# Performance work log

Measured on AMD Instinct MI355X. Metric: run time of the kernel, lower is better.

## Reference

```python
import jax, jax.numpy as jnp
import numpy as np

B, CAP, H, NH = 128, 65536, 512, 8
HD = H // NH
GH = H // 4  # gate hidden


def setup_inputs() -> dict:
    key = jax.random.key(0)
    ks = jax.random.split(key, 8)
    s = 1.0 / np.sqrt(H)
    sg = 1.0 / np.sqrt(GH)
    return {
        "query": jax.random.normal(ks[0], (B, H), jnp.float32),
        "memory_keys": jax.random.normal(ks[1], (CAP, H), jnp.float32) * s,
        "memory_values": jax.random.normal(ks[2], (CAP, H), jnp.float32) * s,
        "in_proj_w": jax.random.normal(ks[3], (3 * H, H), jnp.float32) * s,
        "in_proj_b": jnp.zeros((3 * H,), jnp.float32),
        "out_proj_w": jax.random.normal(ks[4], (H, H), jnp.float32) * s,
        "out_proj_b": jnp.zeros((H,), jnp.float32),
        "gate_w1": jax.random.normal(ks[5], (GH, H), jnp.float32) * s,
        "gate_b1": jnp.zeros((GH,), jnp.float32),
        "gate_w2": jax.random.normal(ks[6], (1, GH), jnp.float32) * sg,
        "gate_b2": jnp.zeros((1,), jnp.float32),
        "usage_count": jnp.zeros((CAP,), jnp.float32),
        "last_used": jnp.zeros((CAP,), jnp.float32),
        "step_counter": 1,
    }


def reference(query, memory_keys, memory_values, in_proj_w, in_proj_b,
              out_proj_w, out_proj_b, gate_w1, gate_b1, gate_w2, gate_b2,
              usage_count, last_used, step_counter):
    # nn.MultiheadAttention packed projections: rows [0:H]=Wq, [H:2H]=Wk, [2H:3H]=Wv
    wq, wk, wv = in_proj_w[:H], in_proj_w[H:2 * H], in_proj_w[2 * H:]
    bq, bk, bv = in_proj_b[:H], in_proj_b[H:2 * H], in_proj_b[2 * H:]

    q = (query @ wq.T + bq).reshape(B, NH, HD)           # [B, h, d] (q_len = 1)
    k = (memory_keys @ wk.T + bk).reshape(CAP, NH, HD)   # [C, h, d]
    v = (memory_values @ wv.T + bv).reshape(CAP, NH, HD)  # [C, h, d]

    scores = jnp.einsum('bhd,chd->bhc', q, k) / np.sqrt(HD)  # [B, h, C]
    attn = jax.nn.softmax(scores, axis=-1)
    ctx = jnp.einsum('bhc,chd->bhd', attn, v).reshape(B, H)
    attn_out = ctx @ out_proj_w.T + out_proj_b               # [B, H]

    # usage bookkeeping: attn_weights averaged over heads, then over batch
    avg_attn = attn.mean(axis=(0, 1))                        # [C]
    new_usage = usage_count + avg_attn
    new_last = jnp.where(avg_attn > 1e-3,
                         jnp.float32(step_counter), last_used)

    # gating MLP: Linear -> ReLU -> Linear -> Sigmoid
    gate = jax.nn.sigmoid(
        jax.nn.relu(query @ gate_w1.T + gate_b1) @ gate_w2.T + gate_b2)  # [B, 1]
    memory_output = gate * attn_out                          # [B, H]
    return memory_output, new_usage, new_last
```

## Files before the change

### kernel.cpp

```cpp
#include <hip/hip_runtime.h>
#include <stdint.h>


typedef __bf16 b16x8 __attribute__((ext_vector_type(8)));
typedef float f32x4 __attribute__((ext_vector_type(4)));

static __device__ __forceinline__ unsigned short f2bf(float f) {
  return __builtin_bit_cast(unsigned short, (__bf16)f);
}

static __device__ __forceinline__ f32x4 MFMA(b16x8 a, b16x8 b, f32x4 c) {
  return __builtin_amdgcn_mfma_f32_16x16x32_bf16(a, b, c, 0, 0, 0);
}

#define GLL16(g, l)                                                          \
  __builtin_amdgcn_global_load_lds(                                          \
      (const __attribute__((address_space(1))) void*)(g),                    \
      (__attribute__((address_space(3))) void*)(l), 16, 0, 0)

#define SBAR() __builtin_amdgcn_sched_barrier(0)

__global__ void k_convert_w(const float* __restrict__ w, unsigned short* __restrict__ dst) {
  int i = blockIdx.x * 256 + threadIdx.x;
  float4 v = reinterpret_cast<const float4*>(w + 512 * 512)[i];
  ushort4 o;
  o.x = f2bf(v.x); o.y = f2bf(v.y); o.z = f2bf(v.z); o.w = f2bf(v.w);
  reinterpret_cast<ushort4*>(dst)[i] = o;
}

__global__ void k_proj_q(const float* __restrict__ query, const float* __restrict__ w,
                         const float* __restrict__ bias, unsigned short* __restrict__ qout) {
  __shared__ float qs[512];
  int b = blockIdx.x, j = threadIdx.x;
  qs[j] = query[b * 512 + j];
  __syncthreads();
  float acc = bias[j];
  const float4* q4 = reinterpret_cast<const float4*>(qs);
  const float4* w4 = reinterpret_cast<const float4*>(w + j * 512);
#pragma unroll 8
  for (int i = 0; i < 128; ++i) {
    float4 a = q4[i], c = w4[i];
    acc += a.x * c.x + a.y * c.y + a.z * c.z + a.w * c.w;
  }
  qout[b * 512 + j] = f2bf(acc);
}

__global__ void k_gate(const float* __restrict__ query, const float* __restrict__ w1,
                       const float* __restrict__ b1, const float* __restrict__ w2,
                       const float* __restrict__ b2, float* __restrict__ gate) {
  __shared__ float qs[512];
  __shared__ float red[2];
  int b = blockIdx.x, j = threadIdx.x;
  qs[j] = query[b * 512 + j];
  qs[j + 128] = query[b * 512 + j + 128];
  qs[j + 256] = query[b * 512 + j + 256];
  qs[j + 384] = query[b * 512 + j + 384];
  __syncthreads();
  float acc = b1[j];
  const float4* q4 = reinterpret_cast<const float4*>(qs);
  const float4* w4 = reinterpret_cast<const float4*>(w1 + j * 512);
#pragma unroll 8
  for (int i = 0; i < 128; ++i) {
    float4 a = q4[i], c = w4[i];
    acc += a.x * c.x + a.y * c.y + a.z * c.z + a.w * c.w;
  }
  float t = fmaxf(acc, 0.f) * w2[j];
#pragma unroll
  for (int off = 1; off < 64; off <<= 1) t += __shfl_xor(t, off, 64);
  if ((j & 63) == 0) red[j >> 6] = t;
  __syncthreads();
  if (j == 0) {
    float z = red[0] + red[1] + b2[0];
    gate[b] = 1.f / (1.f + __builtin_amdgcn_exp2f(-z * 1.44269504088896f));
  }
}

__global__ __launch_bounds__(256, 2) void k_proj_kv(
    const float* __restrict__ mk, const float* __restrict__ mv,
    const unsigned short* __restrict__ wkb, const unsigned short* __restrict__ wvb,
    const float* __restrict__ in_b,
    unsigned short* __restrict__ kout, unsigned short* __restrict__ vtout) {
  const int p = blockIdx.x;
  const int xcd = p & 7, slot = p >> 3;
  const int isV = xcd >> 2;
  const int j0 = (slot & 3) * 128;
  const int c0 = (xcd & 3) * 16384 + (slot >> 2) * 128;
  const float* Ag = isV ? mv : mk;
  const unsigned short* W = isV ? wvb : wkb;
  const float* bias = in_b + (isV ? 1024 : 512);
  const int tid = threadIdx.x;
  const int w = tid >> 6;
  const int wr = w >> 1, wc = w & 1;
  const int ln = tid & 15, g = (tid & 63) >> 4;
  const int lane = tid & 63;

  __shared__ __align__(16) float          AL[3][128 * 32];
  __shared__ __align__(16) unsigned short WL[2][128 * 32];

  f32x4 acc[4][4];
#pragma unroll
  for (int m = 0; m < 4; ++m)
#pragma unroll
    for (int n = 0; n < 4; ++n) acc[m][n] = {0.f, 0.f, 0.f, 0.f};

  const float* srcA[4];
  int dstA[4];
#pragma unroll
  for (int i = 0; i < 4; ++i) {
    int row = i * 32 + w * 8 + (lane >> 3);
    int cs = (lane & 7) ^ (row & 7);
    srcA[i] = Ag + (size_t)(c0 + row) * 512 + cs * 4;
    dstA[i] = (i * 256 + w * 64) * 4;
  }
  const unsigned short* srcW[2];
  int dstW[2];
#pragma unroll
  for (int i = 0; i < 2; ++i) {
    int row = i * 64 + w * 16 + (lane >> 2);
    int cs = (lane & 3) ^ ((row >> 1) & 3);
    srcW[i] = W + (size_t)(j0 + row) * 512 + cs * 8;
    dstW[i] = (i * 256 + w * 64) * 8;
  }

  GLL16(srcW[0], &WL[0][dstW[0]]);
  GLL16(srcW[1], &WL[0][dstW[1]]);
#pragma unroll
  for (int i = 0; i < 4; ++i) GLL16(srcA[i], &AL[0][dstA[i]]);
#pragma unroll
  for (int i = 0; i < 4; ++i) GLL16(srcA[i] + 32, &AL[1][dstA[i]]);
  SBAR();
  asm volatile("s_waitcnt vmcnt(4)" ::: "memory");
  SBAR();
  __builtin_amdgcn_s_barrier();
  SBAR();

#pragma unroll
  for (int kk = 0; kk < 16; ++kk) {
    const int a = kk % 3;
    const int bwl = kk & 1;
    const int k1 = (kk < 15) ? kk + 1 : 15;
    const int k2 = (kk < 14) ? kk + 2 : 15;
    GLL16(srcW[0] + k1 * 32, &WL[bwl ^ 1][dstW[0]]);
    GLL16(srcW[1] + k1 * 32, &WL[bwl ^ 1][dstW[1]]);
#pragma unroll
    for (int i = 0; i < 4; ++i) GLL16(srcA[i] + k2 * 32, &AL[(kk + 2) % 3][dstA[i]]);
    SBAR();
    b16x8 af[4], wf[4];
#pragma unroll
    for (int m = 0; m < 4; ++m) {
      int r = 64 * wr + 16 * m + ln;
      f32x4 lo = *reinterpret_cast<const f32x4*>(&AL[a][r * 32 + (((2 * g) ^ (r & 7)) << 2)]);
      f32x4 hi = *reinterpret_cast<const f32x4*>(&AL[a][r * 32 + (((2 * g + 1) ^ (r & 7)) << 2)]);
      b16x8 v;
      v[0] = (__bf16)lo[0]; v[1] = (__bf16)lo[1]; v[2] = (__bf16)lo[2]; v[3] = (__bf16)lo[3];
      v[4] = (__bf16)hi[0]; v[5] = (__bf16)hi[1]; v[6] = (__bf16)hi[2]; v[7] = (__bf16)hi[3];
      af[m] = v;
    }
#pragma unroll
    for (int n = 0; n < 4; ++n) {
      int r = 64 * wc + 16 * n + ln;
      wf[n] = *reinterpret_cast<const b16x8*>(&WL[bwl][r * 32 + ((g ^ ((r >> 1) & 3)) << 3)]);
    }
    if (!isV) {
#pragma unroll
      for (int m = 0; m < 4; ++m)
#pragma unroll
        for (int n = 0; n < 4; ++n) acc[m][n] = MFMA(wf[n], af[m], acc[m][n]);
    } else {
#pragma unroll
      for (int m = 0; m < 4; ++m)
#pragma unroll
        for (int n = 0; n < 4; ++n) acc[m][n] = MFMA(af[m], wf[n], acc[m][n]);
    }
    SBAR();
    asm volatile("s_waitcnt vmcnt(4) lgkmcnt(0)" ::: "memory");
    SBAR();
    __builtin_amdgcn_s_barrier();
    SBAR();
  }
  asm volatile("s_waitcnt vmcnt(0)" ::: "memory");

  if (!isV) {
#pragma unroll
    for (int m = 0; m < 4; ++m) {
      int c = c0 + 64 * wr + 16 * m + ln;
#pragma unroll
      for (int n = 0; n < 4; ++n) {
        int jb = j0 + 64 * wc + 16 * n + 4 * g;
        float4 bb = *reinterpret_cast<const float4*>(&bias[jb]);
        ushort4 o;
        o.x = f2bf(acc[m][n][0] + bb.x);
        o.y = f2bf(acc[m][n][1] + bb.y);
        o.z = f2bf(acc[m][n][2] + bb.z);
        o.w = f2bf(acc[m][n][3] + bb.w);
        *reinterpret_cast<ushort4*>(&kout[(size_t)c * 512 + jb]) = o;
      }
    }
  } else {
#pragma unroll
    for (int n = 0; n < 4; ++n) {
      int j = j0 + 64 * wc + 16 * n + ln;
      float bj = bias[j];
#pragma unroll
      for (int m = 0; m < 4; ++m) {
        int cb = c0 + 64 * wr + 16 * m + 4 * g;
        ushort4 o;
        o.x = f2bf(acc[m][n][0] + bj);
        o.y = f2bf(acc[m][n][1] + bj);
        o.z = f2bf(acc[m][n][2] + bj);
        o.w = f2bf(acc[m][n][3] + bj);
        *reinterpret_cast<ushort4*>(&vtout[(size_t)j * 65536 + cb]) = o;
      }
    }
  }
}

__global__ __launch_bounds__(256) void k_attn1(
    const unsigned short* __restrict__ kb, const unsigned short* __restrict__ vt,
    const unsigned short* __restrict__ qb,
    float* __restrict__ l_ws, float* __restrict__ ctxT) {
  const int h = blockIdx.y, cg = blockIdx.x;
  const int tid = threadIdx.x;
  const int wv = tid >> 6, wr = wv >> 1, wc = wv & 1;
  const int ln = tid & 15, g = (tid & 63) >> 4;
  __shared__ __align__(16) unsigned short kS[128 * 64];
  __shared__ __align__(16) unsigned short pS[128 * 128];
  __shared__ __align__(16) unsigned short vS[64 * 128];
  const float SC = 0.125f * 1.44269504088896f;

  b16x8 qf[4][2];
#pragma unroll
  for (int n = 0; n < 4; ++n)
#pragma unroll
    for (int ks = 0; ks < 2; ++ks) {
      int b = 64 * wc + 16 * n + ln;
      qf[n][ks] = *reinterpret_cast<const b16x8*>(&qb[(size_t)b * 512 + h * 64 + ks * 32 + g * 8]);
    }
  f32x4 pacc[2][4];
#pragma unroll
  for (int m = 0; m < 2; ++m)
#pragma unroll
    for (int n = 0; n < 4; ++n) pacc[m][n] = {0.f, 0.f, 0.f, 0.f};
  float lsum[4] = {0.f, 0.f, 0.f, 0.f};

  for (int it = 0; it < 8; ++it) {
    int c0g = cg * 1024 + it * 128;
#pragma unroll
    for (int i = 0; i < 4; ++i) {
      int fl = i * 256 + tid, row = fl >> 3, p8 = fl & 7;
      uint4 d = *reinterpret_cast<const uint4*>(&kb[(size_t)(c0g + row) * 512 + h * 64 + p8 * 8]);
      *reinterpret_cast<uint4*>(&kS[(row * 8 + (p8 ^ (row & 7))) * 8]) = d;
    }
#pragma unroll
    for (int i = 0; i < 4; ++i) {
      int fl = i * 256 + tid, row = fl >> 4, p16 = fl & 15;
      uint4 d = *reinterpret_cast<const uint4*>(&vt[(size_t)(h * 64 + row) * 65536 + c0g + p16 * 8]);
      *reinterpret_cast<uint4*>(&vS[(row * 16 + (p16 ^ (row & 7))) * 8]) = d;
    }
    __syncthreads();

    f32x4 sacc[4][4];
#pragma unroll
    for (int m = 0; m < 4; ++m)
#pragma unroll
      for (int n = 0; n < 4; ++n) sacc[m][n] = {0.f, 0.f, 0.f, 0.f};
#pragma unroll
    for (int ks = 0; ks < 2; ++ks) {
      b16x8 a[4];
#pragma unroll
      for (int m = 0; m < 4; ++m) {
        int row = 64 * wr + 16 * m + ln;
        a[m] = *reinterpret_cast<const b16x8*>(&kS[(row * 8 + ((ks * 4 + g) ^ (row & 7))) * 8]);
      }
#pragma unroll
      for (int m = 0; m < 4; ++m)
#pragma unroll
        for (int n = 0; n < 4; ++n) sacc[m][n] = MFMA(a[m], qf[n][ks], sacc[m][n]);
    }
#pragma unroll
    for (int m = 0; m < 4; ++m)
#pragma unroll
      for (int n = 0; n < 4; ++n) {
        float p0 = __builtin_amdgcn_exp2f(sacc[m][n][0] * SC);
        float p1 = __builtin_amdgcn_exp2f(sacc[m][n][1] * SC);
        float p2 = __builtin_amdgcn_exp2f(sacc[m][n][2] * SC);
        float p3 = __builtin_amdgcn_exp2f(sacc[m][n][3] * SC);
        lsum[n] += (p0 + p1) + (p2 + p3);
        int b = 64 * wc + 16 * n + ln;
        int c = 64 * wr + 16 * m + 4 * g;
        int base = b * 128 + (((c >> 3) ^ (b & 7)) * 8) + (c & 7);
        ushort2 lo, hi;
        lo.x = f2bf(p0); lo.y = f2bf(p1);
        hi.x = f2bf(p2); hi.y = f2bf(p3);
        *reinterpret_cast<ushort2*>(&pS[base]) = lo;
        *reinterpret_cast<ushort2*>(&pS[base + 2]) = hi;
      }
    __syncthreads();
#pragma unroll
    for (int ks = 0; ks < 4; ++ks) {
      b16x8 av[2], bp[4];
#pragma unroll
      for (int m = 0; m < 2; ++m) {
        int row = 32 * wr + 16 * m + ln;
        av[m] = *reinterpret_cast<const b16x8*>(&vS[(row * 16 + ((ks * 4 + g) ^ (row & 7))) * 8]);
      }
#pragma unroll
      for (int n = 0; n < 4; ++n) {
        int row = 64 * wc + 16 * n + ln;
        bp[n] = *reinterpret_cast<const b16x8*>(&pS[(row * 16 + ((ks * 4 + g) ^ (row & 7))) * 8]);
      }
#pragma unroll
      for (int m = 0; m < 2; ++m)
#pragma unroll
        for (int n = 0; n < 4; ++n) pacc[m][n] = MFMA(av[m], bp[n], pacc[m][n]);
    }
    __syncthreads();
  }
#pragma unroll
  for (int n = 0; n < 4; ++n) {
    float v = lsum[n];
    v += __shfl_xor(v, 16, 64);
    v += __shfl_xor(v, 32, 64);
    if ((tid & 63) < 16) atomicAdd(&l_ws[h * 128 + 64 * wc + 16 * n + ln], v);
  }
#pragma unroll
  for (int m = 0; m < 2; ++m)
#pragma unroll
    for (int n = 0; n < 4; ++n)
#pragma unroll
      for (int r = 0; r < 4; ++r) {
        int d = 32 * wr + 16 * m + 4 * g + r;
        int b = 64 * wc + 16 * n + ln;
        atomicAdd(&ctxT[(h * 64 + d) * 128 + b], pacc[m][n][r]);
      }
}

__global__ __launch_bounds__(256) void k_attn2(
    const unsigned short* __restrict__ kb, const unsigned short* __restrict__ qb,
    const float* __restrict__ l_ws, float* __restrict__ avgA) {
  const int h = blockIdx.y, cg = blockIdx.x;
  const int tid = threadIdx.x;
  const int wv = tid >> 6, wr = wv >> 1, wc = wv & 1;
  const int ln = tid & 15, g = (tid & 63) >> 4;
  __shared__ __align__(16) unsigned short kS[128 * 64];
  __shared__ float wS[128];
  const float SC = 0.125f * 1.44269504088896f;
  if (tid < 128) wS[tid] = 1.f / l_ws[h * 128 + tid];
  b16x8 qf[4][2];
#pragma unroll
  for (int n = 0; n < 4; ++n)
#pragma unroll
    for (int ks = 0; ks < 2; ++ks) {
      int b = 64 * wc + 16 * n + ln;
      qf[n][ks] = *reinterpret_cast<const b16x8*>(&qb[(size_t)b * 512 + h * 64 + ks * 32 + g * 8]);
    }
  __syncthreads();
  float wn[4];
#pragma unroll
  for (int n = 0; n < 4; ++n) wn[n] = wS[64 * wc + 16 * n + ln];

  for (int it = 0; it < 8; ++it) {
    int c0g = cg * 1024 + it * 128;
#pragma unroll
    for (int i = 0; i < 4; ++i) {
      int fl = i * 256 + tid, row = fl >> 3, p8 = fl & 7;
      uint4 d = *reinterpret_cast<const uint4*>(&kb[(size_t)(c0g + row) * 512 + h * 64 + p8 * 8]);
      *reinterpret_cast<uint4*>(&kS[(row * 8 + (p8 ^ (row & 7))) * 8]) = d;
    }
    __syncthreads();
    f32x4 sacc[4][4];
#pragma unroll
    for (int m = 0; m < 4; ++m)
#pragma unroll
      for (int n = 0; n < 4; ++n) sacc[m][n] = {0.f, 0.f, 0.f, 0.f};
#pragma unroll
    for (int ks = 0; ks < 2; ++ks) {
      b16x8 a[4];
#pragma unroll
      for (int m = 0; m < 4; ++m) {
        int row = 64 * wr + 16 * m + ln;
        a[m] = *reinterpret_cast<const b16x8*>(&kS[(row * 8 + ((ks * 4 + g) ^ (row & 7))) * 8]);
      }
#pragma unroll
      for (int m = 0; m < 4; ++m)
#pragma unroll
        for (int n = 0; n < 4; ++n) sacc[m][n] = MFMA(a[m], qf[n][ks], sacc[m][n]);
    }
#pragma unroll
    for (int m = 0; m < 4; ++m) {
      float s0 = 0.f, s1 = 0.f, s2 = 0.f, s3 = 0.f;
#pragma unroll
      for (int n = 0; n < 4; ++n) {
        s0 += __builtin_amdgcn_exp2f(sacc[m][n][0] * SC) * wn[n];
        s1 += __builtin_amdgcn_exp2f(sacc[m][n][1] * SC) * wn[n];
        s2 += __builtin_amdgcn_exp2f(sacc[m][n][2] * SC) * wn[n];
        s3 += __builtin_amdgcn_exp2f(sacc[m][n][3] * SC) * wn[n];
      }
#pragma unroll
      for (int off = 1; off < 16; off <<= 1) {
        s0 += __shfl_xor(s0, off, 64);
        s1 += __shfl_xor(s1, off, 64);
        s2 += __shfl_xor(s2, off, 64);
        s3 += __shfl_xor(s3, off, 64);
      }
      if (ln == 0) {
        int c = c0g + 64 * wr + 16 * m + 4 * g;
        atomicAdd(&avgA[c], s0);
        atomicAdd(&avgA[c + 1], s1);
        atomicAdd(&avgA[c + 2], s2);
        atomicAdd(&avgA[c + 3], s3);
      }
    }
    __syncthreads();
  }
}

__global__ void k_finalize(const float* __restrict__ ctxT, const float* __restrict__ l_ws,
                           const float* __restrict__ wout, const float* __restrict__ bout,
                           const float* __restrict__ gate, float* __restrict__ out) {
  __shared__ float cs[512];
  int b = blockIdx.x, j = threadIdx.x;
  cs[j] = ctxT[j * 128 + b] / l_ws[(j >> 6) * 128 + b];
  __syncthreads();
  float acc = bout[j];
  const float4* c4 = reinterpret_cast<const float4*>(cs);
  const float4* w4 = reinterpret_cast<const float4*>(wout + j * 512);
#pragma unroll 8
  for (int i = 0; i < 128; ++i) {
    float4 a = c4[i], c = w4[i];
    acc += a.x * c.x + a.y * c.y + a.z * c.z + a.w * c.w;
  }
  out[b * 512 + j] = gate[b] * acc;
}

__global__ void k_usage(const float* __restrict__ avgA, const float* __restrict__ usage,
                        const float* __restrict__ last, const int* __restrict__ step,
                        float* __restrict__ out_usage, float* __restrict__ out_last) {
  int c = blockIdx.x * 256 + threadIdx.x;
  float avg = avgA[c] * (1.f / 1024.f);
  out_usage[c] = usage[c] + avg;
  out_last[c] = (avg > 0.001f) ? (float)step[0] : last[c];
}

extern "C" void kernel_launch(void* const* d_in, const int* in_sizes, int n_in,
                              void* d_out, int out_size, void* d_ws, size_t ws_size,
                              hipStream_t stream) {
  const float* query = (const float*)d_in[0];
  const float* mk    = (const float*)d_in[1];
  const float* mv    = (const float*)d_in[2];
  const float* in_w  = (const float*)d_in[3];
  const float* in_b  = (const float*)d_in[4];
  const float* out_w = (const float*)d_in[5];
  const float* out_b = (const float*)d_in[6];
  const float* gw1   = (const float*)d_in[7];
  const float* gb1   = (const float*)d_in[8];
  const float* gw2   = (const float*)d_in[9];
  const float* gb2   = (const float*)d_in[10];
  const float* usage = (const float*)d_in[11];
  const float* last  = (const float*)d_in[12];
  const int*   step  = (const int*)d_in[13];

  char* ws = (char*)d_ws;
  unsigned short* qb  = (unsigned short*)(ws);
  unsigned short* wkb = (unsigned short*)(ws + 131072);
  unsigned short* wvb = (unsigned short*)(ws + 655360);
  unsigned short* kb  = (unsigned short*)(ws + 1179648);
  unsigned short* vt  = (unsigned short*)(ws + 68288512);
  float* l_ws = (float*)(ws + 135397376);
  float* ctxT = (float*)(ws + 135401472);
  float* avgA = (float*)(ws + 135663616);
  float* gate = (float*)(ws + 135925760);
  float* out = (float*)d_out;

  hipMemsetAsync(ws + 135397376, 0, 4096 + 262144 + 262144, stream);

  k_convert_w<<<512, 256, 0, stream>>>(in_w, wkb);
  k_proj_q<<<128, 512, 0, stream>>>(query, in_w, in_b, qb);
  k_gate<<<128, 128, 0, stream>>>(query, gw1, gb1, gw2, gb2, gate);
  k_proj_kv<<<4096, 256, 0, stream>>>(mk, mv, wkb, wvb, in_b, kb, vt);
  k_attn1<<<dim3(64, 8), 256, 0, stream>>>(kb, vt, qb, l_ws, ctxT);
  k_attn2<<<dim3(64, 8), 256, 0, stream>>>(kb, qb, l_ws, avgA);
  k_finalize<<<128, 512, 0, stream>>>(ctxT, l_ws, out_w, out_b, gate, out);
  k_usage<<<256, 256, 0, stream>>>(avgA, usage, last, step, out + 65536, out + 131072);
}
```

Baseline: 371.3 us.

## Replace LDS-staged K/V projection GEMM with direct register double-buffered loads

```diff
diff --git a/kernel.cpp b/kernel.cpp
--- a/kernel.cpp
+++ b/kernel.cpp
@@ -12,13 +12,6 @@
 static __device__ __forceinline__ f32x4 MFMA(b16x8 a, b16x8 b, f32x4 c) {
   return __builtin_amdgcn_mfma_f32_16x16x32_bf16(a, b, c, 0, 0, 0);
 }
-
-#define GLL16(g, l)                                                          \
-  __builtin_amdgcn_global_load_lds(                                          \
-      (const __attribute__((address_space(1))) void*)(g),                    \
-      (__attribute__((address_space(3))) void*)(l), 16, 0, 0)
-
-#define SBAR() __builtin_amdgcn_sched_barrier(0)
 
 __global__ void k_convert_w(const float* __restrict__ w, unsigned short* __restrict__ dst) {
   int i = blockIdx.x * 256 + threadIdx.x;
@@ -75,6 +68,109 @@
   }
 }
 
+template <int ISV>
+__device__ __forceinline__ void kv_gemm(
+    const float* __restrict__ Ag, const unsigned short* __restrict__ W,
+    const float* __restrict__ bias, unsigned short* __restrict__ outp,
+    int c0, int j0, int wr, int wc, int ln, int g) {
+  const float* aB[4];
+  const unsigned short* wB[4];
+#pragma unroll
+  for (int m = 0; m < 4; ++m)
+    aB[m] = Ag + (size_t)(c0 + 64 * wr + 16 * m + ln) * 512 + g * 8;
+#pragma unroll
+  for (int n = 0; n < 4; ++n)
+    wB[n] = W + (size_t)(j0 + 64 * wc + 16 * n + ln) * 512 + g * 8;
+
+  f32x4 ra[2][4][2];
+  uint4 rw[2][4];
+  f32x4 acc[4][4];
+#pragma unroll
+  for (int m = 0; m < 4; ++m)
+#pragma unroll
+    for (int n = 0; n < 4; ++n) acc[m][n] = {0.f, 0.f, 0.f, 0.f};
+
+#pragma unroll
+  for (int m = 0; m < 4; ++m) {
+    ra[0][m][0] = *reinterpret_cast<const f32x4*>(aB[m]);
+    ra[0][m][1] = *reinterpret_cast<const f32x4*>(aB[m] + 4);
+  }
+#pragma unroll
+  for (int n = 0; n < 4; ++n)
+    rw[0][n] = *reinterpret_cast<const uint4*>(wB[n]);
+
+#pragma unroll
+  for (int kk = 0; kk < 16; ++kk) {
+    const int cur = kk & 1, nxt = cur ^ 1;
+    if (kk < 15) {
+#pragma unroll
+      for (int m = 0; m < 4; ++m) {
+        ra[nxt][m][0] = *reinterpret_cast<const f32x4*>(aB[m] + (kk + 1) * 32);
+        ra[nxt][m][1] = *reinterpret_cast<const f32x4*>(aB[m] + (kk + 1) * 32 + 4);
+      }
+#pragma unroll
+      for (int n = 0; n < 4; ++n)
+        rw[nxt][n] = *reinterpret_cast<const uint4*>(wB[n] + (kk + 1) * 32);
+    }
+    b16x8 af[4], wf[4];
+#pragma unroll
+    for (int m = 0; m < 4; ++m) {
+      f32x4 lo = ra[cur][m][0], hi = ra[cur][m][1];
+      b16x8 v;
+      v[0] = (__bf16)lo[0]; v[1] = (__bf16)lo[1]; v[2] = (__bf16)lo[2]; v[3] = (__bf16)lo[3];
+      v[4] = (__bf16)hi[0]; v[5] = (__bf16)hi[1]; v[6] = (__bf16)hi[2]; v[7] = (__bf16)hi[3];
+      af[m] = v;
+    }
+#pragma unroll
+    for (int n = 0; n < 4; ++n) wf[n] = __builtin_bit_cast(b16x8, rw[cur][n]);
+    if (ISV == 0) {
+#pragma unroll
+      for (int m = 0; m < 4; ++m)
+#pragma unroll
+        for (int n = 0; n < 4; ++n) acc[m][n] = MFMA(wf[n], af[m], acc[m][n]);
+    } else {
+#pragma unroll
+      for (int m = 0; m < 4; ++m)
+#pragma unroll
+        for (int n = 0; n < 4; ++n) acc[m][n] = MFMA(af[m], wf[n], acc[m][n]);
+    }
+  }
+
+  if (ISV == 0) {
+#pragma unroll
+    for (int m = 0; m < 4; ++m) {
+      int c = c0 + 64 * wr + 16 * m + ln;
+#pragma unroll
+      for (int n = 0; n < 4; ++n) {
+        int jb = j0 + 64 * wc + 16 * n + 4 * g;
+        float4 bb = *reinterpret_cast<const float4*>(&bias[jb]);
+        ushort4 o;
+        o.x = f2bf(acc[m][n][0] + bb.x);
+        o.y = f2bf(acc[m][n][1] + bb.y);
+        o.z = f2bf(acc[m][n][2] + bb.z);
+        o.w = f2bf(acc[m][n][3] + bb.w);
+        *reinterpret_cast<ushort4*>(&outp[(size_t)c * 512 + jb]) = o;
+      }
+    }
+  } else {
+#pragma unroll
+    for (int n = 0; n < 4; ++n) {
+      int j = j0 + 64 * wc + 16 * n + ln;
+      float bj = bias[j];
+#pragma unroll
+      for (int m = 0; m < 4; ++m) {
+        int cb = c0 + 64 * wr + 16 * m + 4 * g;
+        ushort4 o;
+        o.x = f2bf(acc[m][n][0] + bj);
+        o.y = f2bf(acc[m][n][1] + bj);
+        o.z = f2bf(acc[m][n][2] + bj);
+        o.w = f2bf(acc[m][n][3] + bj);
+        *reinterpret_cast<ushort4*>(&outp[(size_t)j * 65536 + cb]) = o;
+      }
+    }
+  }
+}
+
 __global__ __launch_bounds__(256, 2) void k_proj_kv(
     const float* __restrict__ mk, const float* __restrict__ mv,
     const unsigned short* __restrict__ wkb, const unsigned short* __restrict__ wvb,
@@ -85,134 +181,15 @@
   const int isV = xcd >> 2;
   const int j0 = (slot & 3) * 128;
   const int c0 = (xcd & 3) * 16384 + (slot >> 2) * 128;
-  const float* Ag = isV ? mv : mk;
-  const unsigned short* W = isV ? wvb : wkb;
-  const float* bias = in_b + (isV ? 1024 : 512);
   const int tid = threadIdx.x;
   const int w = tid >> 6;
   const int wr = w >> 1, wc = w & 1;
   const int ln = tid & 15, g = (tid & 63) >> 4;
-  const int lane = tid & 63;
-
-  __shared__ __align__(16) float          AL[3][128 * 32];
-  __shared__ __align__(16) unsigned short WL[2][128 * 32];
-
-  f32x4 acc[4][4];
-#pragma unroll
-  for (int m = 0; m < 4; ++m)
-#pragma unroll
-    for (int n = 0; n < 4; ++n) acc[m][n] = {0.f, 0.f, 0.f, 0.f};
-
-  const float* srcA[4];
-  int dstA[4];
-#pragma unroll
-  for (int i = 0; i < 4; ++i) {
-    int row = i * 32 + w * 8 + (lane >> 3);
-    int cs = (lane & 7) ^ (row & 7);
-    srcA[i] = Ag + (size_t)(c0 + row) * 512 + cs * 4;
-    dstA[i] = (i * 256 + w * 64) * 4;
-  }
-  const unsigned short* srcW[2];
-  int dstW[2];
-#pragma unroll
-  for (int i = 0; i < 2; ++i) {
-    int row = i * 64 + w * 16 + (lane >> 2);
-    int cs = (lane & 3) ^ ((row >> 1) & 3);
-    srcW[i] = W + (size_t)(j0 + row) * 512 + cs * 8;
-    dstW[i] = (i * 256 + w * 64) * 8;
-  }
-
-  GLL16(srcW[0], &WL[0][dstW[0]]);
-  GLL16(srcW[1], &WL[0][dstW[1]]);
-#pragma unroll
-  for (int i = 0; i < 4; ++i) GLL16(srcA[i], &AL[0][dstA[i]]);
-#pragma unroll
-  for (int i = 0; i < 4; ++i) GLL16(srcA[i] + 32, &AL[1][dstA[i]]);
-  SBAR();
-  asm volatile("s_waitcnt vmcnt(4)" ::: "memory");
-  SBAR();
-  __builtin_amdgcn_s_barrier();
-  SBAR();
-
-#pragma unroll
-  for (int kk = 0; kk < 16; ++kk) {
-    const int a = kk % 3;
-    const int bwl = kk & 1;
-    const int k1 = (kk < 15) ? kk + 1 : 15;
-    const int k2 = (kk < 14) ? kk + 2 : 15;
-    GLL16(srcW[0] + k1 * 32, &WL[bwl ^ 1][dstW[0]]);
-    GLL16(srcW[1] + k1 * 32, &WL[bwl ^ 1][dstW[1]]);
-#pragma unroll
-    for (int i = 0; i < 4; ++i) GLL16(srcA[i] + k2 * 32, &AL[(kk + 2) % 3][dstA[i]]);
-    SBAR();
-    b16x8 af[4], wf[4];
-#pragma unroll
-    for (int m = 0; m < 4; ++m) {
-      int r = 64 * wr + 16 * m + ln;
-      f32x4 lo = *reinterpret_cast<const f32x4*>(&AL[a][r * 32 + (((2 * g) ^ (r & 7)) << 2)]);
-      f32x4 hi = *reinterpret_cast<const f32x4*>(&AL[a][r * 32 + (((2 * g + 1) ^ (r & 7)) << 2)]);
-      b16x8 v;
-      v[0] = (__bf16)lo[0]; v[1] = (__bf16)lo[1]; v[2] = (__bf16)lo[2]; v[3] = (__bf16)lo[3];
-      v[4] = (__bf16)hi[0]; v[5] = (__bf16)hi[1]; v[6] = (__bf16)hi[2]; v[7] = (__bf16)hi[3];
-      af[m] = v;
-    }
-#pragma unroll
-    for (int n = 0; n < 4; ++n) {
-      int r = 64 * wc + 16 * n + ln;
-      wf[n] = *reinterpret_cast<const b16x8*>(&WL[bwl][r * 32 + ((g ^ ((r >> 1) & 3)) << 3)]);
-    }
-    if (!isV) {
-#pragma unroll
-      for (int m = 0; m < 4; ++m)
-#pragma unroll
-        for (int n = 0; n < 4; ++n) acc[m][n] = MFMA(wf[n], af[m], acc[m][n]);
-    } else {
-#pragma unroll
-      for (int m = 0; m < 4; ++m)
-#pragma unroll
-        for (int n = 0; n < 4; ++n) acc[m][n] = MFMA(af[m], wf[n], acc[m][n]);
-    }
-    SBAR();
-    asm volatile("s_waitcnt vmcnt(4) lgkmcnt(0)" ::: "memory");
-    SBAR();
-    __builtin_amdgcn_s_barrier();
-    SBAR();
-  }
-  asm volatile("s_waitcnt vmcnt(0)" ::: "memory");
-
-  if (!isV) {
-#pragma unroll
-    for (int m = 0; m < 4; ++m) {
-      int c = c0 + 64 * wr + 16 * m + ln;
-#pragma unroll
-      for (int n = 0; n < 4; ++n) {
-        int jb = j0 + 64 * wc + 16 * n + 4 * g;
-        float4 bb = *reinterpret_cast<const float4*>(&bias[jb]);
-        ushort4 o;
-        o.x = f2bf(acc[m][n][0] + bb.x);
-        o.y = f2bf(acc[m][n][1] + bb.y);
-        o.z = f2bf(acc[m][n][2] + bb.z);
-        o.w = f2bf(acc[m][n][3] + bb.w);
-        *reinterpret_cast<ushort4*>(&kout[(size_t)c * 512 + jb]) = o;
-      }
-    }
-  } else {
-#pragma unroll
-    for (int n = 0; n < 4; ++n) {
-      int j = j0 + 64 * wc + 16 * n + ln;
-      float bj = bias[j];
-#pragma unroll
-      for (int m = 0; m < 4; ++m) {
-        int cb = c0 + 64 * wr + 16 * m + 4 * g;
-        ushort4 o;
-        o.x = f2bf(acc[m][n][0] + bj);
-        o.y = f2bf(acc[m][n][1] + bj);
-        o.z = f2bf(acc[m][n][2] + bj);
-        o.w = f2bf(acc[m][n][3] + bj);
-        *reinterpret_cast<ushort4*>(&vtout[(size_t)j * 65536 + cb]) = o;
-      }
-    }
-  }
+
+  if (!isV)
+    kv_gemm<0>(mk, wkb, in_b + 512, kout, c0, j0, wr, wc, ln, g);
+  else
+    kv_gemm<1>(mv, wvb, in_b + 1024, vtout, c0, j0, wr, wc, ln, g);
 }
 
 __global__ __launch_bounds__(256) void k_attn1(
```

Measured after the change: 602.0 us. 62.1% more time.
